# Optimization experiments

Hardware: AMD Instinct MI355X
Metric: run time of the kernel (lower is better)

## Reference

```python
import jax, jax.numpy as jnp
import numpy as np

B, SEQ, C, H = 4, 1024, 256, 4
Dk = C // H                                  # 64
L = 4 * SEQ                                  # 4096 attention length
FACTOR = 4
N_TOP = FACTOR * int(np.ceil(np.log(L)))     # U = 36 dominant queries
SAMPLE_K = FACTOR * int(np.ceil(np.log(L)))  # u = 36 sampled keys per query


def _forward(et, mp, co, vol, Wq, bq, Wk, bk, Wv, bv, Wo, bo, index_sample):
    sz = et.shape[0]
    # student_graph input shuffle (faithful to the torch .view calls)
    x = jnp.concatenate([et.reshape(SEQ, -1), co.reshape(SEQ, -1),
                         mp.reshape(SEQ, -1), vol.reshape(SEQ, -1)], axis=-1)
    x = x.reshape(sz, L, C)  # [B, 4*seq_len, d_model]
    # projections; ProbAttention uses view(B,H,L,-1) which is a raw reshape
    # (NOT a transpose) of the [B,L,H,Dk] tensor -> fuse into one reshape
    q = (x @ Wq + bq).reshape(sz, H, L, Dk)
    k = (x @ Wk + bk).reshape(sz, H, L, Dk)
    v = (x @ Wv + bv).reshape(sz, H, L, Dk)
    # _prob_QK: random key sampling + sparsity measure + top-k query select
    K_sample = k[:, :, index_sample, :]                        # [B,H,L,u,Dk]
    QKs = jnp.einsum('bhse,bhske->bhsk', q, K_sample)          # [B,H,L,u]
    M = QKs.max(axis=-1) - QKs.sum(axis=-1) / L                # [B,H,L]
    _, m_top = jax.lax.top_k(M, N_TOP)                         # [B,H,U]
    q_red = jnp.take_along_axis(q, m_top[..., None], axis=2)   # [B,H,U,Dk]
    scores = jnp.einsum('bhue,bhle->bhul', q_red, k) * (1.0 / float(np.sqrt(Dk)))
    attn = jax.nn.softmax(scores, axis=-1)                     # [B,H,U,L]
    upd = jnp.einsum('bhul,bhld->bhud', attn, v)               # [B,H,U,Dk]
    # initial context = V-sum broadcast; scatter dense update at top queries
    ctx = jnp.broadcast_to(v.sum(axis=2, keepdims=True), (sz, H, L, Dk))
    bi = jnp.arange(sz)[:, None, None]
    hi = jnp.arange(H)[None, :, None]
    ctx = ctx.at[bi, hi, m_top, :].set(upd)                    # [B,H,L,Dk]
    # AttentionLayer output: .view(B, L, -1) on contiguous [B,H,L,Dk] is again
    # a raw reshape (faithful), then out projection
    out = ctx.reshape(sz, L, H * Dk) @ Wo + bo                 # [B,L,C]
    return out.reshape(SEQ, -1)


def setup_inputs():
    key = jax.random.key(0)
    ks = jax.random.split(key, 13)
    f = lambda i, shp: jax.random.normal(ks[i], shp, jnp.float32)
    ws = 1.0 / float(np.sqrt(C))  # keep logits in a sane range
    return {
        'et': f(0, (B, SEQ, C)), 'mp': f(1, (B, SEQ, C)),
        'co': f(2, (B, SEQ, C)), 'vol': f(3, (B, SEQ, C)),
        'Wq': f(4, (C, C)) * ws, 'bq': f(5, (C,)) * 0.01,
        'Wk': f(6, (C, C)) * ws, 'bk': f(7, (C,)) * 0.01,
        'Wv': f(8, (C, C)) * ws, 'bv': f(9, (C,)) * 0.01,
        'Wo': f(10, (C, C)) * ws, 'bo': f(11, (C,)) * 0.01,
        'index_sample': jax.random.randint(ks[12], (L, SAMPLE_K), 0, L, dtype=jnp.int32),
        'comp_idx': 0,
    }


def reference(et, mp, co, vol, Wq, bq, Wk, bk, Wv, bv, Wo, bo, index_sample, comp_idx):
    return _forward(et, mp, co, vol, Wq, bq, Wk, bk, Wv, bv, Wo, bo, index_sample)
```

## Files before the change

kernel.cpp:

```cpp
#include <hip/hip_runtime.h>
#include <hip/hip_bf16.h>

#define BHn 16
#define Ln 4096
#define NTOP 36
#define SKn 36
#define NCHUNK 64

using s16x8 = __attribute__((ext_vector_type(8))) short;
using u16x8 = __attribute__((ext_vector_type(8))) unsigned short;
using f32x4 = __attribute__((ext_vector_type(4))) float;

__device__ __forceinline__ unsigned short bf_hi(float f) {
  unsigned u = __float_as_uint(f);
  return (unsigned short)((u + 0x7fffu + ((u >> 16) & 1u)) >> 16);
}

__global__ __launch_bounds__(256) void wxconv(
    const float* __restrict__ W0, const float* __restrict__ W1, const float* __restrict__ W2,
    unsigned short* __restrict__ th0, unsigned short* __restrict__ tl0,
    unsigned short* __restrict__ th1, unsigned short* __restrict__ tl1,
    unsigned short* __restrict__ th2, unsigned short* __restrict__ tl2,
    const float* __restrict__ s0, const float* __restrict__ s1,
    const float* __restrict__ s2, const float* __restrict__ s3,
    unsigned short* __restrict__ Axh, unsigned short* __restrict__ Axl) {
  int bx = blockIdx.x;
  int t = threadIdx.x;
  if (bx < 48) {
    int wsel = bx >> 4;
    const float* W = (wsel == 0) ? W0 : (wsel == 1) ? W1 : W2;
    unsigned short* TH = (wsel == 0) ? th0 : (wsel == 1) ? th1 : th2;
    unsigned short* TL = (wsel == 0) ? tl0 : (wsel == 1) ? tl1 : tl2;
    int kr = (bx & 15) * 16;
    int n = t;
    u16x8 hv[2], lv[2];
#pragma unroll
    for (int j = 0; j < 16; ++j) {
      float f = W[(size_t)(kr + j) * 256 + n];
      unsigned short h = bf_hi(f);
      float lof = f - __uint_as_float(((unsigned)h) << 16);
      hv[j >> 3][j & 7] = h;
      lv[j >> 3][j & 7] = bf_hi(lof);
    }
    *(u16x8*)&TH[(size_t)n * 256 + kr] = hv[0];
    *(u16x8*)&TH[(size_t)n * 256 + kr + 8] = hv[1];
    *(u16x8*)&TL[(size_t)n * 256 + kr] = lv[0];
    *(u16x8*)&TL[(size_t)n * 256 + kr + 8] = lv[1];
  } else {
    int row = (bx - 48) * 4 + (t >> 6);
    int c = t & 63;
    int l = row & 4095, b = row >> 12;
    int part = (l >> 2) & 3;
    int seq = ((l >> 4) << 2) | (l & 3);
    const float* sp = (part == 0) ? s0 : (part == 1) ? s1 : (part == 2) ? s2 : s3;
    float4 f = ((const float4*)(sp + (size_t)((b << 10) + seq) * 256))[c];
    float fv[4] = {f.x, f.y, f.z, f.w};
    ushort4 hv, lv;
    unsigned short* hp = (unsigned short*)&hv;
    unsigned short* lp = (unsigned short*)&lv;
#pragma unroll
    for (int j = 0; j < 4; ++j) {
      unsigned short h = bf_hi(fv[j]);
      float lof = fv[j] - __uint_as_float(((unsigned)h) << 16);
      hp[j] = h;
      lp[j] = bf_hi(lof);
    }
    *(ushort4*)&Axh[(size_t)row * 256 + c * 4] = hv;
    *(ushort4*)&Axl[(size_t)row * 256 + c * 4] = lv;
  }
}

#define LDW 40
__global__ __launch_bounds__(256, 3) void qkv_mfma(
    const unsigned short* __restrict__ Axh, const unsigned short* __restrict__ Axl,
    const unsigned short* __restrict__ th0, const unsigned short* __restrict__ tl0,
    const unsigned short* __restrict__ th1, const unsigned short* __restrict__ tl1,
    const unsigned short* __restrict__ th2, const unsigned short* __restrict__ tl2,
    const float* __restrict__ b0, const float* __restrict__ b1, const float* __restrict__ b2,
    float* __restrict__ o0, float* __restrict__ o1, float* __restrict__ o2) {
  __shared__ __align__(16) unsigned short Ah[128 * LDW];
  __shared__ __align__(16) unsigned short Al[128 * LDW];
  __shared__ __align__(16) unsigned short Bh[128 * LDW];
  __shared__ __align__(16) unsigned short Bl[128 * LDW];
  int t = threadIdx.x;
  int g = blockIdx.x;
  int vnt = g >> 7;
  int wsel = vnt >> 1;
  int col0 = (vnt & 1) * 128;
  int row0 = (g & 127) * 128;
  const unsigned short* TH = (wsel == 0) ? th0 : (wsel == 1) ? th1 : th2;
  const unsigned short* TL = (wsel == 0) ? tl0 : (wsel == 1) ? tl1 : tl2;
  const float* bias = (wsel == 0) ? b0 : (wsel == 1) ? b1 : b2;
  float* O = (wsel == 0) ? o0 : (wsel == 1) ? o1 : o2;
  const bool vlite = (wsel == 2);

  int srow = t >> 1, half = t & 1;
  const unsigned short* ah_g = Axh + (size_t)(row0 + srow) * 256 + half * 16;
  const unsigned short* al_g = Axl + (size_t)(row0 + srow) * 256 + half * 16;
  const unsigned short* bh_g = TH + (size_t)(col0 + srow) * 256 + half * 16;
  const unsigned short* bl_g = TL + (size_t)(col0 + srow) * 256 + half * 16;

  int lane = t & 63;
  int wv = t >> 6;
  int wr = wv >> 1, wc = wv & 1;
  int fr = lane & 15, fk = lane >> 4;
  int aoff = (wr * 64 + fr) * LDW + fk * 8;
  int boff = (wc * 64 + fr) * LDW + fk * 8;

  f32x4 acc[4][4] = {};

  for (int k0 = 0; k0 < 256; k0 += 32) {
    int wa = srow * LDW + half * 16;
    u16x8 va0 = *(const u16x8*)(ah_g + k0);
    u16x8 va1 = *(const u16x8*)(ah_g + k0 + 8);
    u16x8 vb0 = *(const u16x8*)(bh_g + k0);
    u16x8 vb1 = *(const u16x8*)(bh_g + k0 + 8);
    *(u16x8*)&Ah[wa] = va0; *(u16x8*)&Ah[wa + 8] = va1;
    *(u16x8*)&Bh[wa] = vb0; *(u16x8*)&Bh[wa + 8] = vb1;
    if (!vlite) {
      u16x8 vl0 = *(const u16x8*)(al_g + k0);
      u16x8 vl1 = *(const u16x8*)(al_g + k0 + 8);
      u16x8 vc0 = *(const u16x8*)(bl_g + k0);
      u16x8 vc1 = *(const u16x8*)(bl_g + k0 + 8);
      *(u16x8*)&Al[wa] = vl0; *(u16x8*)&Al[wa + 8] = vl1;
      *(u16x8*)&Bl[wa] = vc0; *(u16x8*)&Bl[wa + 8] = vc1;
    }
    __syncthreads();

    if (vlite) {
      s16x8 fah[4];
#pragma unroll
      for (int mi = 0; mi < 4; ++mi)
        fah[mi] = *(const s16x8*)&Ah[aoff + mi * 16 * LDW];
#pragma unroll
      for (int ni = 0; ni < 4; ++ni) {
        s16x8 fbh = *(const s16x8*)&Bh[boff + ni * 16 * LDW];
#pragma unroll
        for (int mi = 0; mi < 4; ++mi)
          acc[mi][ni] = __builtin_amdgcn_mfma_f32_16x16x32_bf16(fah[mi], fbh, acc[mi][ni], 0, 0, 0);
      }
    } else {
      s16x8 fah[4], fal[4];
#pragma unroll
      for (int mi = 0; mi < 4; ++mi) {
        fah[mi] = *(const s16x8*)&Ah[aoff + mi * 16 * LDW];
        fal[mi] = *(const s16x8*)&Al[aoff + mi * 16 * LDW];
      }
#pragma unroll
      for (int ni = 0; ni < 4; ++ni) {
        s16x8 fbh = *(const s16x8*)&Bh[boff + ni * 16 * LDW];
        s16x8 fbl = *(const s16x8*)&Bl[boff + ni * 16 * LDW];
#pragma unroll
        for (int mi = 0; mi < 4; ++mi) {
          acc[mi][ni] = __builtin_amdgcn_mfma_f32_16x16x32_bf16(fah[mi], fbh, acc[mi][ni], 0, 0, 0);
          acc[mi][ni] = __builtin_amdgcn_mfma_f32_16x16x32_bf16(fal[mi], fbh, acc[mi][ni], 0, 0, 0);
          acc[mi][ni] = __builtin_amdgcn_mfma_f32_16x16x32_bf16(fah[mi], fbl, acc[mi][ni], 0, 0, 0);
        }
      }
    }
    __syncthreads();
  }

#pragma unroll
  for (int ni = 0; ni < 4; ++ni) {
    int n = col0 + wc * 64 + ni * 16 + fr;
    float bv = bias[n];
#pragma unroll
    for (int mi = 0; mi < 4; ++mi) {
      int mb = row0 + wr * 64 + mi * 16 + fk * 4;
#pragma unroll
      for (int r = 0; r < 4; ++r)
        O[(size_t)(mb + r) * 256 + n] = acc[mi][ni][r] + bv;
    }
  }
}

__global__ __launch_bounds__(256) void qks_m3(
    const float* __restrict__ q, const float* __restrict__ k,
    const int* __restrict__ idxs, float* __restrict__ Mout) {
  __shared__ float qs[64][68];
  __shared__ int il[64 * SKn];
  int g = blockIdx.x;
  int x = g & 7;
  int i = g >> 3;
  int bh = (x << 1) | (i >> 6);
  int s0 = (i & 63) * 64;
  int t = threadIdx.x;
  size_t base = (size_t)bh << 12;
  for (int i2 = t; i2 < 1024; i2 += 256) {
    int row = i2 >> 4, d4 = i2 & 15;
    *(float4*)&qs[row][d4 * 4] = ((const float4*)(q + (base + s0 + row) * 64))[d4];
  }
  for (int i2 = t; i2 < 64 * SKn; i2 += 256) il[i2] = idxs[s0 * SKn + i2];
  __syncthreads();
  int sl = t >> 2;
  int dq = t & 3;
  float qr[16];
#pragma unroll
  for (int i2 = 0; i2 < 4; ++i2)
    *(float4*)&qr[i2 * 4] = *(const float4*)&qs[sl][i2 * 16 + dq * 4];
  float mx = -INFINITY, sm = 0.f;
  const float4* kb4 = (const float4*)(k + base * 64);
#pragma unroll 8
  for (int j = 0; j < SKn; ++j) {
    int l = il[sl * SKn + j];
    const float4* kr = kb4 + (size_t)l * 16;
    float acc = 0.f;
#pragma unroll
    for (int i2 = 0; i2 < 4; ++i2) {
      float4 kv = kr[i2 * 4 + dq];
      acc += kv.x * qr[i2 * 4] + kv.y * qr[i2 * 4 + 1] + kv.z * qr[i2 * 4 + 2] + kv.w * qr[i2 * 4 + 3];
    }
    acc += __shfl_xor(acc, 1, 64);
    acc += __shfl_xor(acc, 2, 64);
    mx = fmaxf(mx, acc);
    sm += acc;
  }
  if (dq == 0) Mout[base + s0 + sl] = mx - sm * (1.0f / 4096.0f);
}

__global__ __launch_bounds__(256) void topk_radix(
    const float* __restrict__ M, int* __restrict__ topidx) {
  __shared__ unsigned hist[4096];
  __shared__ unsigned sup[256];
  __shared__ unsigned cand_u[256];
  __shared__ int cand_i[256];
  __shared__ int s_bin1, s_bin2, s_above, s_ocnt, s_ccnt;
  int bh = blockIdx.x;
  int t = threadIdx.x;
  int mbase = bh * 4096;
  unsigned uv[16];
  for (int i = t; i < 4096; i += 256) hist[i] = 0;
  __syncthreads();
#pragma unroll
  for (int r = 0; r < 16; ++r) {
    unsigned b = __float_as_uint(M[mbase + t + 256 * r]);
    unsigned u = b ^ ((unsigned)((int)b >> 31) | 0x80000000u);
    uv[r] = u;
    atomicAdd(&hist[u >> 20], 1u);
  }
  __syncthreads();
  {
    unsigned ssum = 0;
    for (int i = 0; i < 16; ++i) ssum += hist[t * 16 + i];
    sup[t] = ssum;
  }
  __syncthreads();
  if (t == 0) {
    unsigned cum = 0; int sb = 255;
    for (; sb > 0; --sb) { if (cum + sup[sb] >= NTOP) break; cum += sup[sb]; }
    int b = sb * 16 + 15;
    for (; b > sb * 16; --b) { if (cum + hist[b] >= NTOP) break; cum += hist[b]; }
    s_bin1 = b; s_above = (int)cum;
  }
  __syncthreads();
  int bin1 = s_bin1;
  int need1 = NTOP - s_above;
  __syncthreads();
  for (int i = t; i < 4096; i += 256) hist[i] = 0;
  __syncthreads();
#pragma unroll
  for (int r = 0; r < 16; ++r)
    if ((int)(uv[r] >> 20) == bin1) atomicAdd(&hist[(uv[r] >> 8) & 0xFFF], 1u);
  __syncthreads();
  {
    unsigned ssum = 0;
    for (int i = 0; i < 16; ++i) ssum += hist[t * 16 + i];
    sup[t] = ssum;
  }
  __syncthreads();
  if (t == 0) {
    unsigned cum = 0; int sb = 255;
    for (; sb > 0; --sb) { if (cum + sup[sb] >= (unsigned)need1) break; cum += sup[sb]; }
    int b = sb * 16 + 15;
    for (; b > sb * 16; --b) { if (cum + hist[b] >= (unsigned)need1) break; cum += hist[b]; }
    s_bin2 = b; s_above += (int)cum;
    s_ocnt = 0; s_ccnt = 0;
  }
  __syncthreads();
  int bin2 = s_bin2;
  int need = NTOP - s_above;
  int* outp = topidx + bh * NTOP;
#pragma unroll
  for (int r = 0; r < 16; ++r) {
    unsigned u = uv[r];
    int b1 = u >> 20, b2 = (u >> 8) & 0xFFF;
    if (b1 > bin1 || (b1 == bin1 && b2 > bin2)) {
      int p = atomicAdd(&s_ocnt, 1);
      outp[p] = t + 256 * r;
    } else if (b1 == bin1 && b2 == bin2) {
      int p = atomicAdd(&s_ccnt, 1);
      if (p < 256) { cand_u[p] = u; cand_i[p] = t + 256 * r; }
    }
  }
  __syncthreads();
  if (t == 0) {
    int cc = s_ccnt < 256 ? s_ccnt : 256;
    int slot = s_ocnt;
    for (int n = 0; n < need; ++n) {
      unsigned bu = 0; int bi = 0x7fffffff, bp = -1;
      for (int c = 0; c < cc; ++c) {
        if (cand_i[c] < 0) continue;
        if (cand_u[c] > bu || (cand_u[c] == bu && cand_i[c] < bi)) {
          bu = cand_u[c]; bi = cand_i[c]; bp = c;
        }
      }
      outp[slot++] = bi;
      cand_i[bp] = -1;
    }
  }
}

__global__ __launch_bounds__(256) void attn_partial(
    const float* __restrict__ q, const float* __restrict__ k,
    const float* __restrict__ v, const int* __restrict__ topidx,
    float* __restrict__ part_m, float* __restrict__ part_s,
    unsigned short* __restrict__ part_ob, float* __restrict__ vpart2) {
  __shared__ float4 Ks4[64][17];
  __shared__ float4 qs4[36][17];
  __shared__ float S[36][68];
  int g = blockIdx.x;
  int x = g & 7;
  int i = g >> 3;
  int bh = (x << 1) | (i >> 6);
  int c = i & 63;
  int l0 = c * 64;
  int t = threadIdx.x;
  size_t base = (size_t)bh * 4096;

  const float4* kg = (const float4*)(k + (base + l0) * 64);
  for (int i2 = t; i2 < 64 * 16; i2 += 256) {
    int row = i2 >> 4, d4 = i2 & 15;
    Ks4[row][d4] = kg[row * 16 + d4];
  }
  for (int i2 = t; i2 < 36 * 16; i2 += 256) {
    int u = i2 >> 4, d4 = i2 & 15;
    int m = topidx[bh * NTOP + u];
    qs4[u][d4] = ((const float4*)(q + (base + m) * 64))[d4];
  }
  __syncthreads();

  {
    int l = t & 63, ug = t >> 6;
    float acc[9] = {};
#pragma unroll
    for (int d4 = 0; d4 < 16; ++d4) {
      float4 kv = Ks4[l][d4];
#pragma unroll
      for (int j = 0; j < 9; ++j) {
        float4 qv = qs4[ug * 9 + j][d4];
        acc[j] += kv.x * qv.x + kv.y * qv.y + kv.z * qv.z + kv.w * qv.w;
      }
    }
#pragma unroll
    for (int j = 0; j < 9; ++j) S[ug * 9 + j][l] = acc[j] * 0.125f;
  }
  __syncthreads();

  if (t < 144) {
    int u = t >> 2, p = t & 3;
    int lb = p * 16;
    float mx = -INFINITY;
#pragma unroll
    for (int l2 = 0; l2 < 16; ++l2) mx = fmaxf(mx, S[u][lb + l2]);
    mx = fmaxf(mx, __shfl_xor(mx, 1, 64));
    mx = fmaxf(mx, __shfl_xor(mx, 2, 64));
    float sm = 0.f;
#pragma unroll
    for (int l2 = 0; l2 < 16; ++l2) {
      float e = expf(S[u][lb + l2] - mx);
      S[u][lb + l2] = e;
      sm += e;
    }
    sm += __shfl_xor(sm, 1, 64);
    sm += __shfl_xor(sm, 2, 64);
    if (p == 0) {
      part_m[((size_t)bh * NCHUNK + c) * NTOP + u] = mx;
      part_s[((size_t)bh * NCHUNK + c) * NTOP + u] = sm;
    }
  }
  __syncthreads();

  {
    int d = t & 63, ug = t >> 6;
    float pacc[9] = {};
    float vs = 0.f;
    const float* vg = v + (base + l0) * 64;
    for (int l = 0; l < 64; ++l) {
      float vv = vg[l * 64 + d];
      vs += vv;
#pragma unroll
      for (int j = 0; j < 9; ++j) pacc[j] += S[ug * 9 + j][l] * vv;
    }
#pragma unroll
    for (int j = 0; j < 9; ++j)
      part_ob[(((size_t)bh * NCHUNK + c) * NTOP + ug * 9 + j) * 64 + d] = bf_hi(pacc[j]);
    if (ug == 0) vpart2[((size_t)bh * NCHUNK + c) * 64 + d] = vs;
  }
}

__global__ __launch_bounds__(256) void vsum_out(
    const float* __restrict__ vpart2, const float* __restrict__ Wo,
    const float* __restrict__ bo, float* __restrict__ vsum,
    float* __restrict__ outbase) {
  __shared__ float red[4][64];
  __shared__ float vs[64];
  int bh = blockIdx.x;
  int t = threadIdx.x;
  int d = t & 63, qq = t >> 6;
  float acc = 0.f;
  for (int c = qq; c < NCHUNK; c += 4)
    acc += vpart2[((size_t)bh * NCHUNK + c) * 64 + d];
  red[qq][d] = acc;
  __syncthreads();
  if (qq == 0) {
    float s = red[0][d] + red[1][d] + red[2][d] + red[3][d];
    vs[d] = s;
    vsum[bh * 64 + d] = s;
  }
  __syncthreads();
  float ob = bo[t];
#pragma unroll 8
  for (int dd = 0; dd < 64; ++dd) {
    float w4 = Wo[dd * 256 + t] + Wo[(64 + dd) * 256 + t] +
               Wo[(128 + dd) * 256 + t] + Wo[(192 + dd) * 256 + t];
    ob += vs[dd] * w4;
  }
  outbase[bh * 256 + t] = ob;
}

__global__ __launch_bounds__(256) void out_fill(
    const float* __restrict__ outbase, float4* __restrict__ out4) {
  int g = blockIdx.x * 256 + threadIdx.x;
  int c4 = g & 63;
  int bh = g >> 16;
  out4[g] = ((const float4*)outbase)[bh * 64 + c4];
}

__global__ __launch_bounds__(256) void combine_patch(
    const float* __restrict__ part_m, const float* __restrict__ part_s,
    const unsigned short* __restrict__ part_ob, const float* __restrict__ vsum,
    const int* __restrict__ topidx, const float* __restrict__ Wo,
    float* __restrict__ out) {
  __shared__ float wl[64];
  __shared__ float red[4][64];
  __shared__ float dv[64];
  __shared__ float ds_s;
  int widx = blockIdx.x;
  int bh = widx / NTOP;
  int u = widx % NTOP;
  int t = threadIdx.x;
  int d = t & 63, qq = t >> 6;
  if (t < 64) {
    float m_c = part_m[((size_t)bh * NCHUNK + t) * NTOP + u];
    float M = m_c;
#pragma unroll
    for (int off = 32; off > 0; off >>= 1) M = fmaxf(M, __shfl_xor(M, off, 64));
    float w = expf(m_c - M);
    float ds = part_s[((size_t)bh * NCHUNK + t) * NTOP + u] * w;
#pragma unroll
    for (int off = 32; off > 0; off >>= 1) ds += __shfl_xor(ds, off, 64);
    wl[t] = w;
    if (t == 0) ds_s = ds;
  }
  __syncthreads();
  float acc = 0.f;
#pragma unroll
  for (int j = 0; j < 16; ++j) {
    int c = qq + j * 4;
    float po = __uint_as_float(
        ((unsigned)part_ob[(((size_t)bh * NCHUNK + c) * NTOP + u) * 64 + d]) << 16);
    acc += po * wl[c];
  }
  red[qq][d] = acc;
  __syncthreads();
  if (qq == 0)
    dv[d] = (red[0][d] + red[1][d] + red[2][d] + red[3][d]) / ds_s - vsum[bh * 64 + d];
  __syncthreads();
  int m = topidx[widx];
  int h = bh & 3, b = bh >> 2;
  int j2 = m & 3;
  int lp = h * 1024 + (m >> 2);
  float acc2 = 0.f;
#pragma unroll 8
  for (int dd = 0; dd < 64; ++dd) acc2 += dv[dd] * Wo[(j2 * 64 + dd) * 256 + t];
  atomicAdd(&out[((size_t)(b * 4096 + lp)) * 256 + t], acc2);
}

extern "C" void kernel_launch(void* const* d_in, const int* in_sizes, int n_in,
                              void* d_out, int out_size, void* d_ws, size_t ws_size,
                              hipStream_t stream) {
  const float* et  = (const float*)d_in[0];
  const float* mp  = (const float*)d_in[1];
  const float* co  = (const float*)d_in[2];
  const float* vol = (const float*)d_in[3];
  const float* Wq = (const float*)d_in[4];
  const float* bq = (const float*)d_in[5];
  const float* Wk = (const float*)d_in[6];
  const float* bk = (const float*)d_in[7];
  const float* Wv = (const float*)d_in[8];
  const float* bv = (const float*)d_in[9];
  const float* Wo = (const float*)d_in[10];
  const float* bo = (const float*)d_in[11];
  const int* idxs = (const int*)d_in[12];
  float* out = (float*)d_out;

  char* ws = (char*)d_ws;
  const size_t BIG = 16u * 1024u * 1024u;
  float* qb = (float*)(ws);
  float* kb = (float*)(ws + BIG);
  float* vb = (float*)(ws + 2 * BIG);
  char* sm = ws + 3 * BIG;
  float* Mbuf   = (float*)(sm);
  int*   topidx = (int*)(sm + 262144);
  float* vsum   = (float*)(sm + 262144 + 4096);
  char* pm = sm + 262144 + 4096 + 8192;
  float* part_m = (float*)(pm);
  float* part_s = (float*)(pm + 147456);
  unsigned short* part_ob = (unsigned short*)(pm + 2 * 147456);
  float* outbase = (float*)(pm + 2 * 147456 + 4718592);
  unsigned short* wt = (unsigned short*)(pm + 2 * 147456 + 4718592 + 16384);
  unsigned short* wth0 = wt;
  unsigned short* wtl0 = wt + 65536;
  unsigned short* wth1 = wt + 2 * 65536;
  unsigned short* wtl1 = wt + 3 * 65536;
  unsigned short* wth2 = wt + 4 * 65536;
  unsigned short* wtl2 = wt + 5 * 65536;
  unsigned short* axh = wt + 6 * 65536;
  unsigned short* axl = axh + 16384 * 256;
  float* vpart2 = (float*)(axl + 16384 * 256);

  wxconv<<<4144, 256, 0, stream>>>(Wq, Wk, Wv, wth0, wtl0, wth1, wtl1, wth2, wtl2,
                                   et, co, mp, vol, axh, axl);

  qkv_mfma<<<768, 256, 0, stream>>>(
      axh, axl, wth0, wtl0, wth1, wtl1, wth2, wtl2, bq, bk, bv, qb, kb, vb);

  qks_m3<<<1024, 256, 0, stream>>>(qb, kb, idxs, Mbuf);

  topk_radix<<<BHn, 256, 0, stream>>>(Mbuf, topidx);

  attn_partial<<<1024, 256, 0, stream>>>(
      qb, kb, vb, topidx, part_m, part_s, part_ob, vpart2);

  vsum_out<<<BHn, 256, 0, stream>>>(vpart2, Wo, bo, vsum, outbase);

  out_fill<<<4096, 256, 0, stream>>>(outbase, (float4*)out);

  combine_patch<<<BHn * NTOP, 256, 0, stream>>>(
      part_m, part_s, part_ob, vsum, topidx, Wo, out);
}
```

Baseline: 129.0 us.

## Load QKV GEMM MFMA fragments directly from global memory, dropping LDS staging

The QKV projection GEMM no longer stages A and B tiles through shared memory with barriers. Each wave instead loads its bf16 hi/lo MFMA fragments straight from global memory, and the k-loop is unrolled by two. This removes the LDS writes, LDS reads and __syncthreads, but the two waves that share a row or column tile now each fetch the same data from global/L2. The occupancy hint of 3 blocks per SM is also dropped.

```diff
diff --git a/kernel.cpp b/kernel.cpp
--- a/kernel.cpp
+++ b/kernel.cpp
@@ -70,18 +70,13 @@
   }
 }
 
-#define LDW 40
-__global__ __launch_bounds__(256, 3) void qkv_mfma(
+__global__ __launch_bounds__(256) void qkv_mfma(
     const unsigned short* __restrict__ Axh, const unsigned short* __restrict__ Axl,
     const unsigned short* __restrict__ th0, const unsigned short* __restrict__ tl0,
     const unsigned short* __restrict__ th1, const unsigned short* __restrict__ tl1,
     const unsigned short* __restrict__ th2, const unsigned short* __restrict__ tl2,
     const float* __restrict__ b0, const float* __restrict__ b1, const float* __restrict__ b2,
     float* __restrict__ o0, float* __restrict__ o1, float* __restrict__ o2) {
-  __shared__ __align__(16) unsigned short Ah[128 * LDW];
-  __shared__ __align__(16) unsigned short Al[128 * LDW];
-  __shared__ __align__(16) unsigned short Bh[128 * LDW];
-  __shared__ __align__(16) unsigned short Bl[128 * LDW];
   int t = threadIdx.x;
   int g = blockIdx.x;
   int vnt = g >> 7;
@@ -94,71 +89,59 @@
   float* O = (wsel == 0) ? o0 : (wsel == 1) ? o1 : o2;
   const bool vlite = (wsel == 2);
 
-  int srow = t >> 1, half = t & 1;
-  const unsigned short* ah_g = Axh + (size_t)(row0 + srow) * 256 + half * 16;
-  const unsigned short* al_g = Axl + (size_t)(row0 + srow) * 256 + half * 16;
-  const unsigned short* bh_g = TH + (size_t)(col0 + srow) * 256 + half * 16;
-  const unsigned short* bl_g = TL + (size_t)(col0 + srow) * 256 + half * 16;
-
   int lane = t & 63;
   int wv = t >> 6;
   int wr = wv >> 1, wc = wv & 1;
   int fr = lane & 15, fk = lane >> 4;
-  int aoff = (wr * 64 + fr) * LDW + fk * 8;
-  int boff = (wc * 64 + fr) * LDW + fk * 8;
+
+  const unsigned short* aph[4];
+  const unsigned short* apl[4];
+  const unsigned short* bph[4];
+  const unsigned short* bpl[4];
+#pragma unroll
+  for (int mi = 0; mi < 4; ++mi) {
+    size_t arow = (size_t)(row0 + wr * 64 + mi * 16 + fr) * 256 + fk * 8;
+    aph[mi] = Axh + arow;
+    apl[mi] = Axl + arow;
+    size_t brow = (size_t)(col0 + wc * 64 + mi * 16 + fr) * 256 + fk * 8;
+    bph[mi] = TH + brow;
+    bpl[mi] = TL + brow;
+  }
 
   f32x4 acc[4][4] = {};
 
+#pragma unroll 2
   for (int k0 = 0; k0 < 256; k0 += 32) {
-    int wa = srow * LDW + half * 16;
-    u16x8 va0 = *(const u16x8*)(ah_g + k0);
-    u16x8 va1 = *(const u16x8*)(ah_g + k0 + 8);
-    u16x8 vb0 = *(const u16x8*)(bh_g + k0);
-    u16x8 vb1 = *(const u16x8*)(bh_g + k0 + 8);
-    *(u16x8*)&Ah[wa] = va0; *(u16x8*)&Ah[wa + 8] = va1;
-    *(u16x8*)&Bh[wa] = vb0; *(u16x8*)&Bh[wa + 8] = vb1;
-    if (!vlite) {
-      u16x8 vl0 = *(const u16x8*)(al_g + k0);
-      u16x8 vl1 = *(const u16x8*)(al_g + k0 + 8);
-      u16x8 vc0 = *(const u16x8*)(bl_g + k0);
-      u16x8 vc1 = *(const u16x8*)(bl_g + k0 + 8);
-      *(u16x8*)&Al[wa] = vl0; *(u16x8*)&Al[wa + 8] = vl1;
-      *(u16x8*)&Bl[wa] = vc0; *(u16x8*)&Bl[wa + 8] = vc1;
-    }
-    __syncthreads();
-
     if (vlite) {
-      s16x8 fah[4];
-#pragma unroll
-      for (int mi = 0; mi < 4; ++mi)
-        fah[mi] = *(const s16x8*)&Ah[aoff + mi * 16 * LDW];
-#pragma unroll
-      for (int ni = 0; ni < 4; ++ni) {
-        s16x8 fbh = *(const s16x8*)&Bh[boff + ni * 16 * LDW];
+      s16x8 fah[4], fbh[4];
+#pragma unroll
+      for (int mi = 0; mi < 4; ++mi) {
+        fah[mi] = *(const s16x8*)(aph[mi] + k0);
+        fbh[mi] = *(const s16x8*)(bph[mi] + k0);
+      }
+#pragma unroll
+      for (int ni = 0; ni < 4; ++ni)
 #pragma unroll
         for (int mi = 0; mi < 4; ++mi)
-          acc[mi][ni] = __builtin_amdgcn_mfma_f32_16x16x32_bf16(fah[mi], fbh, acc[mi][ni], 0, 0, 0);
+          acc[mi][ni] = __builtin_amdgcn_mfma_f32_16x16x32_bf16(fah[mi], fbh[ni], acc[mi][ni], 0, 0, 0);
+    } else {
+      s16x8 fah[4], fal[4], fbh[4], fbl[4];
+#pragma unroll
+      for (int mi = 0; mi < 4; ++mi) {
+        fah[mi] = *(const s16x8*)(aph[mi] + k0);
+        fal[mi] = *(const s16x8*)(apl[mi] + k0);
+        fbh[mi] = *(const s16x8*)(bph[mi] + k0);
+        fbl[mi] = *(const s16x8*)(bpl[mi] + k0);
       }
-    } else {
-      s16x8 fah[4], fal[4];
-#pragma unroll
-      for (int mi = 0; mi < 4; ++mi) {
-        fah[mi] = *(const s16x8*)&Ah[aoff + mi * 16 * LDW];
-        fal[mi] = *(const s16x8*)&Al[aoff + mi * 16 * LDW];
-      }
-#pragma unroll
-      for (int ni = 0; ni < 4; ++ni) {
-        s16x8 fbh = *(const s16x8*)&Bh[boff + ni * 16 * LDW];
-        s16x8 fbl = *(const s16x8*)&Bl[boff + ni * 16 * LDW];
+#pragma unroll
+      for (int ni = 0; ni < 4; ++ni)
 #pragma unroll
         for (int mi = 0; mi < 4; ++mi) {
-          acc[mi][ni] = __builtin_amdgcn_mfma_f32_16x16x32_bf16(fah[mi], fbh, acc[mi][ni], 0, 0, 0);
-          acc[mi][ni] = __builtin_amdgcn_mfma_f32_16x16x32_bf16(fal[mi], fbh, acc[mi][ni], 0, 0, 0);
-          acc[mi][ni] = __builtin_amdgcn_mfma_f32_16x16x32_bf16(fah[mi], fbl, acc[mi][ni], 0, 0, 0);
+          acc[mi][ni] = __builtin_amdgcn_mfma_f32_16x16x32_bf16(fah[mi], fbh[ni], acc[mi][ni], 0, 0, 0);
+          acc[mi][ni] = __builtin_amdgcn_mfma_f32_16x16x32_bf16(fal[mi], fbh[ni], acc[mi][ni], 0, 0, 0);
+          acc[mi][ni] = __builtin_amdgcn_mfma_f32_16x16x32_bf16(fah[mi], fbl[ni], acc[mi][ni], 0, 0, 0);
         }
-      }
-    }
-    __syncthreads();
+    }
   }
 
 #pragma unroll
```

Measured after the change: 155.5 us. +20.5%, slower.
